# Kernel tuning notes

Measured on AMD Instinct MI355X. Metric: run time of the kernel, lower is better.

Reference implementation:

```python
import jax, jax.numpy as jnp
import numpy as np

CUTOFF = 3.5
EPS = 1e-7  # keras.backend.epsilon()


def triplet_indices(N):
    # All triplets (i, j, k) with j < k and j, k != i  -> [N, T, 3], T = (N-1)(N-2)/2
    idx = []
    for i in range(N):
        others = [a for a in range(N) if a != i]
        for a in range(len(others)):
            for b in range(a + 1, len(others)):
                idx.append((i, others[a], others[b]))
    T = (N - 1) * (N - 2) // 2
    return np.asarray(idx, dtype=np.int32).reshape(N, T, 3)


def f_C(distance):
    return 0.5 * jnp.cos(np.pi * distance / CUTOFF) + 0.5


def _he(key, shape):
    fan_in = shape[0]
    return jax.random.normal(key, shape, dtype=jnp.float32) * np.sqrt(2.0 / fan_in)


def setup_inputs() -> dict:
    key = jax.random.key(0)
    ks = jax.random.split(key, 10)
    B, N = 32, 32
    # build realistic symmetric distance matrices from random coordinates
    coords = jax.random.normal(ks[0], (B, N, 3), dtype=jnp.float32) * 2.0
    D = jnp.linalg.norm(coords[:, :, None, :] - coords[:, None, :, :], axis=-1)
    Z = jax.random.randint(ks[1], (B, N), 1, 10).astype(jnp.float32)
    dims = [(9, 64), (64, 64), (64, 64), (64, 64), (64, 64), (64, 128), (128, 256)]
    inp = {"distance_matrices": D, "num_species_batch": Z}
    for li, (fi, fo) in enumerate(dims):
        inp[f"W{li}"] = _he(ks[2 + li], (fi, fo))
        inp[f"b{li}"] = jnp.zeros((fo,), dtype=jnp.float32)
    return inp


def ang_mlp(x, W0, b0, W1, b1, W2, b2, W3, b3, W4, b4, W5, b5, W6, b6):
    x_res = jnp.tanh(x @ W0 + b0)
    h = jnp.tanh(x_res @ W1 + b1)
    blk1 = h + x_res
    h = jnp.tanh(blk1 @ W2 + b2)
    h = jnp.tanh(h @ W3 + b3)
    h = jnp.tanh(h @ W4 + b4)
    blk2 = h + blk1
    blk3 = jnp.tanh(blk2 @ W5 + b5)
    return jnp.tanh(blk3 @ W6 + b6)


def reference(distance_matrices, num_species_batch, W0, b0, W1, b1, W2, b2,
              W3, b3, W4, b4, W5, b5, W6, b6):
    D = distance_matrices          # [B, N, N]
    Z = num_species_batch          # [B, N]
    N = D.shape[1]
    trip = jnp.asarray(triplet_indices(N))          # [N, T, 3] static
    ti, tj, tk = trip[..., 0], trip[..., 1], trip[..., 2]   # each [N, T]

    # gather triplet distances / species -> [B, N, T]
    R_ij = D[:, ti, tj]
    R_ik = D[:, ti, tk]
    R_jk = D[:, tj, tk]
    z_i, z_j, z_k = Z[:, ti], Z[:, tj], Z[:, tk]

    # Carnot formula for angles
    def carnot(a, b, c):
        return (a ** 2 + b ** 2 - c ** 2) / jnp.maximum(2.0 * a * b, 1e-10)
    cos_i = carnot(R_ij, R_ik, R_jk)
    cos_j = carnot(R_ij, R_jk, R_ik)
    cos_k = carnot(R_ik, R_jk, R_ij)

    geo = jnp.stack([R_ij + R_ik + R_jk,
                     R_ij * R_ik + R_ij * R_jk + R_ik * R_jk,
                     R_ij * R_ik * R_jk], axis=-1)                      # [B,N,T,3]
    chem = jnp.stack([
        z_i + z_j + z_k,
        cos_i + cos_j + cos_k,
        z_i * (z_j + z_k) + z_j * z_k - cos_i * (cos_j + cos_k) - cos_j * cos_k,
        z_i * (cos_j + cos_k) + cos_i * (z_j + z_k) + z_j * cos_k + cos_j * z_k,
        z_i * (z_j * z_k - cos_j * cos_k) - cos_i * (z_j * cos_k + cos_j * z_k),
        z_i * (z_j * cos_k + cos_j * z_k) + cos_i * (z_j * z_k - cos_j * cos_k),
    ], axis=-1)                                                          # [B,N,T,6]
    geo = geo / (jnp.linalg.norm(geo, axis=-1, keepdims=True) + EPS)
    chem = chem / (jnp.linalg.norm(chem, axis=-1, keepdims=True) + EPS)
    mlp_in = jnp.concatenate([geo, chem], axis=-1)                       # [B,N,T,9]

    mlp_out = ang_mlp(mlp_in, W0, b0, W1, b1, W2, b2, W3, b3, W4, b4, W5, b5, W6, b6)  # [B,N,T,256]

    # cutoff smoothing; triplets with a central distance beyond the cutoff map to 0
    within = ((R_ij < CUTOFF) & (R_ik < CUTOFF)).astype(mlp_out.dtype)
    smooth = f_C(R_ij) * f_C(R_ik) * within                              # [B,N,T]
    aev = jnp.sum(mlp_out * smooth[..., None], axis=2)                   # [B,N,256]
    return aev
```

## Files before the change

kernel.cpp:

```cpp
#include <hip/hip_runtime.h>

namespace {

constexpr int T = 465;
constexpr int M = 31;
constexpr float FCUT = 3.5f;
constexpr float PI_OVER_CUT = 0.8975979010256552f;
constexpr int REC = 12;
constexpr int K2_BLOCKS = 512;
constexpr int MAXROWS_HARD = 1024 * 480;

constexpr int OFF_WB = 0;
constexpr int OFF_B  = 4096;
constexpr int OFF_A  = 8192;
constexpr int OFF_C  = 12288;
constexpr int OFF_F  = 16384;
constexpr int OFF_SM = 16960;
constexpr int OFF_CT = 17024;
constexpr int LDS_FLOATS = 17088;

__device__ __forceinline__ float ftanh(float x) {
    x = fminf(fmaxf(x, -15.0f), 15.0f);
    const float e = __expf(2.0f * x);
    return (e - 1.0f) * __builtin_amdgcn_rcpf(e + 1.0f);
}

__global__ __launch_bounds__(64, 1)
void feat_kernel(const float* __restrict__ D, const float* __restrict__ Z,
                 float* __restrict__ rows, int* __restrict__ ctr, int maxrows)
{
    const int lane = threadIdx.x;
    const int center = blockIdx.x;
    const int bi = center >> 5, i = center & 31;
    const float* __restrict__ Drow = D + bi * 1024;
    const float* __restrict__ Zrow = Z + bi * 32;
    const float z_i = Zrow[i];

    unsigned long long masks[8];
    int cnt = 0;
    #pragma unroll
    for (int rnd = 0; rnd < 8; ++rnd) {
        const int t = rnd * 64 + lane;
        bool act = false;
        if (t < T) {
            int a = 0, rem = t;
            while (rem >= M - 1 - a) { rem -= M - 1 - a; ++a; }
            const int b = a + 1 + rem;
            const int j = a + (a >= i);
            const int k = b + (b >= i);
            const float rij = Drow[i * 32 + j];
            const float rik = Drow[i * 32 + k];
            act = (rij < FCUT) && (rik < FCUT);
        }
        masks[rnd] = __ballot(act);
        cnt += (int)__popcll(masks[rnd]);
    }
    const int padded = (cnt + 15) & ~15;
    if (padded == 0) return;
    int base = 0;
    if (lane == 0) base = atomicAdd(ctr, padded);
    base = __shfl(base, 0);
    if (base + padded > maxrows) return;

    int pre = 0;
    #pragma unroll
    for (int rnd = 0; rnd < 8; ++rnd) {
        const unsigned long long mb = masks[rnd];
        const bool act = (mb >> lane) & 1ull;
        const int slot = base + pre + (int)__popcll(mb & ((1ull << lane) - 1ull));
        pre += (int)__popcll(mb);
        if (act) {
            const int t = rnd * 64 + lane;
            int a = 0, rem = t;
            while (rem >= M - 1 - a) { rem -= M - 1 - a; ++a; }
            const int b = a + 1 + rem;
            const int j = a + (a >= i);
            const int k = b + (b >= i);
            const float rij = Drow[i * 32 + j];
            const float rik = Drow[i * 32 + k];
            const float rjk = Drow[j * 32 + k];
            const float zj = Zrow[j], zk = Zrow[k];
            const float rij2 = rij * rij, rik2 = rik * rik, rjk2 = rjk * rjk;
            const float ci = (rij2 + rik2 - rjk2) / fmaxf(2.f * rij * rik, 1e-10f);
            const float cj = (rij2 + rjk2 - rik2) / fmaxf(2.f * rij * rjk, 1e-10f);
            const float ck = (rik2 + rjk2 - rij2) / fmaxf(2.f * rik * rjk, 1e-10f);
            const float g0 = rij + rik + rjk;
            const float g1 = rij * rik + rij * rjk + rik * rjk;
            const float g2 = rij * rik * rjk;
            const float rg = 1.0f / (sqrtf(g0 * g0 + g1 * g1 + g2 * g2) + 1e-7f);
            const float s0 = z_i + zj + zk;
            const float s1 = ci + cj + ck;
            const float s2 = z_i * (zj + zk) + zj * zk - ci * (cj + ck) - cj * ck;
            const float s3 = z_i * (cj + ck) + ci * (zj + zk) + zj * ck + cj * zk;
            const float s4 = z_i * (zj * zk - cj * ck) - ci * (zj * ck + cj * zk);
            const float s5 = z_i * (zj * ck + cj * zk) + ci * (zj * zk - cj * ck);
            const float rs = 1.0f / (sqrtf(s0*s0 + s1*s1 + s2*s2 + s3*s3 + s4*s4 + s5*s5) + 1e-7f);
            const float fij = 0.5f * cosf(PI_OVER_CUT * rij) + 0.5f;
            const float fik = 0.5f * cosf(PI_OVER_CUT * rik) + 0.5f;
            float4* dst = (float4*)(rows + (size_t)slot * REC);
            dst[0] = make_float4(g0 * rg, g1 * rg, g2 * rg, s0 * rs);
            dst[1] = make_float4(s1 * rs, s2 * rs, s3 * rs, s4 * rs);
            dst[2] = make_float4(s5 * rs, fij * fik, __int_as_float(center), 0.f);
        }
    }
    for (int p = cnt + lane; p < padded; p += 64) {
        float4* dst = (float4*)(rows + (size_t)(base + p) * REC);
        dst[0] = make_float4(0.f, 0.f, 0.f, 0.f);
        dst[1] = make_float4(0.f, 0.f, 0.f, 0.f);
        dst[2] = make_float4(0.f, 0.f, __int_as_float(center), 0.f);
    }
}

template<int INF>
__device__ __forceinline__ void stage_w(const float* __restrict__ W, int OUT, int c0,
                                        float* __restrict__ wb, int t)
{
    constexpr int TOT = INF * 64 / 4;
    #pragma unroll 1
    for (int idx = t; idx < TOT; idx += 256) {
        const int f = idx * 4;
        const int kk = f >> 6;
        const int c = f & 63;
        *(float4*)(wb + f) = *(const float4*)(W + (size_t)kk * OUT + c0 + c);
    }
}

template<int INF>
__device__ __forceinline__ void accum(const float* __restrict__ wb,
                                      const float* __restrict__ xin,
                                      int lane, int wcol, float acc[16])
{
    #pragma unroll 4
    for (int kk = 0; kk < INF; ++kk) {
        const float x = xin[kk * 64 + lane];
        const float* wr = wb + kk * 64 + wcol;
        const float4 w0 = *(const float4*)(wr + 0);
        const float4 w1 = *(const float4*)(wr + 4);
        const float4 w2 = *(const float4*)(wr + 8);
        const float4 w3 = *(const float4*)(wr + 12);
        acc[ 0] = fmaf(x, w0.x, acc[ 0]);  acc[ 1] = fmaf(x, w0.y, acc[ 1]);
        acc[ 2] = fmaf(x, w0.z, acc[ 2]);  acc[ 3] = fmaf(x, w0.w, acc[ 3]);
        acc[ 4] = fmaf(x, w1.x, acc[ 4]);  acc[ 5] = fmaf(x, w1.y, acc[ 5]);
        acc[ 6] = fmaf(x, w1.z, acc[ 6]);  acc[ 7] = fmaf(x, w1.w, acc[ 7]);
        acc[ 8] = fmaf(x, w2.x, acc[ 8]);  acc[ 9] = fmaf(x, w2.y, acc[ 9]);
        acc[10] = fmaf(x, w2.z, acc[10]);  acc[11] = fmaf(x, w2.w, acc[11]);
        acc[12] = fmaf(x, w3.x, acc[12]);  acc[13] = fmaf(x, w3.y, acc[13]);
        acc[14] = fmaf(x, w3.z, acc[14]);  acc[15] = fmaf(x, w3.w, acc[15]);
    }
}

__device__ __forceinline__ void bias_init(const float* __restrict__ Bp, int off,
                                          float acc[16])
{
    const float4 b0 = *(const float4*)(Bp + off + 0);
    const float4 b1 = *(const float4*)(Bp + off + 4);
    const float4 b2 = *(const float4*)(Bp + off + 8);
    const float4 b3 = *(const float4*)(Bp + off + 12);
    acc[0]=b0.x; acc[1]=b0.y; acc[2]=b0.z; acc[3]=b0.w;
    acc[4]=b1.x; acc[5]=b1.y; acc[6]=b1.z; acc[7]=b1.w;
    acc[8]=b2.x; acc[9]=b2.y; acc[10]=b2.z; acc[11]=b2.w;
    acc[12]=b3.x; acc[13]=b3.y; acc[14]=b3.z; acc[15]=b3.w;
}

__global__ __launch_bounds__(256, 2)
void mlp_kernel(const float* __restrict__ rows, const int* __restrict__ ctr,
                const float* __restrict__ W0, const float* __restrict__ B0,
                const float* __restrict__ W1, const float* __restrict__ B1,
                const float* __restrict__ W2, const float* __restrict__ B2,
                const float* __restrict__ W3, const float* __restrict__ B3,
                const float* __restrict__ W4, const float* __restrict__ B4,
                const float* __restrict__ W5, const float* __restrict__ B5,
                const float* __restrict__ W6, const float* __restrict__ B6,
                float* __restrict__ out, int maxrows)
{
    __shared__ float lds[LDS_FLOATS];
    float* __restrict__ WB = lds + OFF_WB;
    float* __restrict__ Bb = lds + OFF_B;
    float* __restrict__ Ab = lds + OFF_A;
    float* __restrict__ Cb = lds + OFF_C;
    float* __restrict__ Fb = lds + OFF_F;
    float* __restrict__ SMb = lds + OFF_SM;
    int*   __restrict__ CTb = (int*)(lds + OFF_CT);

    const int t = threadIdx.x;
    const int lane = t & 63;
    const int wcol = (t >> 6) * 16;
    int nrows = *ctr;
    if (nrows > maxrows) nrows = maxrows & ~15;

    for (int tile = blockIdx.x; tile * 64 < nrows; tile += K2_BLOCKS) {
        __syncthreads();
        if (t < 64) {
            const int r = tile * 64 + t;
            float4 v0 = make_float4(0,0,0,0), v1 = v0, v2 = v0;
            if (r < nrows) {
                const float4* rec = (const float4*)(rows + (size_t)r * REC);
                v0 = rec[0]; v1 = rec[1]; v2 = rec[2];
            } else {
                v2.z = __int_as_float(-1);
            }
            Fb[0*64+t]=v0.x; Fb[1*64+t]=v0.y; Fb[2*64+t]=v0.z;
            Fb[3*64+t]=v0.w; Fb[4*64+t]=v1.x; Fb[5*64+t]=v1.y;
            Fb[6*64+t]=v1.z; Fb[7*64+t]=v1.w; Fb[8*64+t]=v2.x;
            SMb[t] = v2.y;
            CTb[t] = __float_as_int(v2.z);
        }
        stage_w<9>(W0, 64, 0, WB, t);
        __syncthreads();

        float acc[16];

        bias_init(B0, wcol, acc);
        accum<9>(WB, Fb, lane, wcol, acc);
        #pragma unroll
        for (int q = 0; q < 16; ++q) Ab[(wcol + q) * 64 + lane] = ftanh(acc[q]);

        __syncthreads();
        stage_w<64>(W1, 64, 0, WB, t);
        __syncthreads();
        bias_init(B1, wcol, acc);
        accum<64>(WB, Ab, lane, wcol, acc);
        #pragma unroll
        for (int q = 0; q < 16; ++q) {
            const int f = (wcol + q) * 64 + lane;
            Bb[f] = ftanh(acc[q]) + Ab[f];
        }

        __syncthreads();
        stage_w<64>(W2, 64, 0, WB, t);
        __syncthreads();
        bias_init(B2, wcol, acc);
        accum<64>(WB, Bb, lane, wcol, acc);
        #pragma unroll
        for (int q = 0; q < 16; ++q) Cb[(wcol + q) * 64 + lane] = ftanh(acc[q]);

        __syncthreads();
        stage_w<64>(W3, 64, 0, WB, t);
        __syncthreads();
        bias_init(B3, wcol, acc);
        accum<64>(WB, Cb, lane, wcol, acc);
        #pragma unroll
        for (int q = 0; q < 16; ++q) Ab[(wcol + q) * 64 + lane] = ftanh(acc[q]);

        __syncthreads();
        stage_w<64>(W4, 64, 0, WB, t);
        __syncthreads();
        bias_init(B4, wcol, acc);
        accum<64>(WB, Ab, lane, wcol, acc);
        #pragma unroll
        for (int q = 0; q < 16; ++q) {
            const int f = (wcol + q) * 64 + lane;
            Bb[f] = ftanh(acc[q]) + Bb[f];
        }

        __syncthreads();
        stage_w<64>(W5, 128, 0, WB, t);
        __syncthreads();
        bias_init(B5, wcol, acc);
        accum<64>(WB, Bb, lane, wcol, acc);
        #pragma unroll
        for (int q = 0; q < 16; ++q) Ab[(wcol + q) * 64 + lane] = ftanh(acc[q]);

        __syncthreads();
        stage_w<64>(W5, 128, 64, WB, t);
        __syncthreads();
        bias_init(B5, 64 + wcol, acc);
        accum<64>(WB, Bb, lane, wcol, acc);
        #pragma unroll
        for (int q = 0; q < 16; ++q) Cb[(wcol + q) * 64 + lane] = ftanh(acc[q]);

        const float sm = SMb[lane];
        const int ct = CTb[lane];
        #pragma unroll 1
        for (int c0 = 0; c0 < 256; c0 += 64) {
            __syncthreads();
            stage_w<128>(W6, 256, c0, lds, t);
            __syncthreads();
            float a6[16];
            bias_init(B6, c0 + wcol, a6);
            accum<64>(lds, Ab, lane, wcol, a6);
            accum<64>(lds + 64 * 64, Cb, lane, wcol, a6);
            #pragma unroll
            for (int q = 0; q < 16; ++q) {
                float v = ftanh(a6[q]) * sm;
                v += __shfl_xor(v, 1);
                v += __shfl_xor(v, 2);
                v += __shfl_xor(v, 4);
                v += __shfl_xor(v, 8);
                if (((lane & 15) == 0) && ct >= 0)
                    atomicAdd(out + (size_t)ct * 256 + c0 + wcol + q, v);
            }
        }
    }
}

}

extern "C" void kernel_launch(void* const* d_in, const int* in_sizes, int n_in,
                              void* d_out, int out_size, void* d_ws, size_t ws_size,
                              hipStream_t stream) {
    (void)in_sizes; (void)n_in;

    const float* D  = (const float*)d_in[0];
    const float* Z  = (const float*)d_in[1];
    const float* W0 = (const float*)d_in[2];  const float* B0 = (const float*)d_in[3];
    const float* W1 = (const float*)d_in[4];  const float* B1 = (const float*)d_in[5];
    const float* W2 = (const float*)d_in[6];  const float* B2 = (const float*)d_in[7];
    const float* W3 = (const float*)d_in[8];  const float* B3 = (const float*)d_in[9];
    const float* W4 = (const float*)d_in[10]; const float* B4 = (const float*)d_in[11];
    const float* W5 = (const float*)d_in[12]; const float* B5 = (const float*)d_in[13];
    const float* W6 = (const float*)d_in[14]; const float* B6 = (const float*)d_in[15];
    float* out = (float*)d_out;

    int* ctr = (int*)d_ws;
    float* rowbuf = (float*)((char*)d_ws + 64);
    size_t avail = (ws_size > 64) ? (ws_size - 64) / (REC * sizeof(float)) : 0;
    int maxrows = (int)((avail < (size_t)MAXROWS_HARD) ? avail : (size_t)MAXROWS_HARD);

    hipMemsetAsync(d_ws, 0, 64, stream);
    hipMemsetAsync(d_out, 0, sizeof(float) * (size_t)out_size, stream);

    feat_kernel<<<1024, 64, 0, stream>>>(D, Z, rowbuf, ctr, maxrows);
    mlp_kernel<<<K2_BLOCKS, 256, 0, stream>>>(rowbuf, ctr,
                                              W0, B0, W1, B1, W2, B2, W3, B3,
                                              W4, B4, W5, B5, W6, B6, out, maxrows);
}
```

Baseline: 412.9 us.

## Read MLP weights via scalar constant loads instead of staging through LDS

Removes the per-layer staging of weight tiles into shared memory and the barriers around it. Each wave instead reads its 16-column weight slice straight from global memory through the constant address space, with a wave-uniform column index (readfirstlane) so the loads can become scalar loads. The smaller LDS footprint and a launch bound of 3 blocks per CU aim to raise occupancy. In exchange, every k step issues scalar memory loads that depend on the scalar cache, which may add latency compared with LDS reads.

```diff
diff --git a/kernel.cpp b/kernel.cpp
--- a/kernel.cpp
+++ b/kernel.cpp
@@ -10,14 +10,8 @@
 constexpr int K2_BLOCKS = 512;
 constexpr int MAXROWS_HARD = 1024 * 480;
 
-constexpr int OFF_WB = 0;
-constexpr int OFF_B  = 4096;
-constexpr int OFF_A  = 8192;
-constexpr int OFF_C  = 12288;
-constexpr int OFF_F  = 16384;
-constexpr int OFF_SM = 16960;
-constexpr int OFF_CT = 17024;
-constexpr int LDS_FLOATS = 17088;
+typedef float __attribute__((ext_vector_type(4))) f4v;
+typedef const __attribute__((address_space(4))) f4v* cf4p;
 
 __device__ __forceinline__ float ftanh(float x) {
     x = fminf(fmaxf(x, -15.0f), 15.0f);
@@ -111,33 +105,19 @@
     }
 }
 
-template<int INF>
-__device__ __forceinline__ void stage_w(const float* __restrict__ W, int OUT, int c0,
-                                        float* __restrict__ wb, int t)
+template<int INF, int LDW>
+__device__ __forceinline__ void accum_s(const float* Wcol,
+                                        const float* __restrict__ xin,
+                                        int lane, float acc[16])
 {
-    constexpr int TOT = INF * 64 / 4;
-    #pragma unroll 1
-    for (int idx = t; idx < TOT; idx += 256) {
-        const int f = idx * 4;
-        const int kk = f >> 6;
-        const int c = f & 63;
-        *(float4*)(wb + f) = *(const float4*)(W + (size_t)kk * OUT + c0 + c);
-    }
-}
-
-template<int INF>
-__device__ __forceinline__ void accum(const float* __restrict__ wb,
-                                      const float* __restrict__ xin,
-                                      int lane, int wcol, float acc[16])
-{
-    #pragma unroll 4
+    cf4p w = (cf4p)(uintptr_t)Wcol;
+    #pragma unroll 2
     for (int kk = 0; kk < INF; ++kk) {
+        const f4v w0 = w[kk * (LDW / 4) + 0];
+        const f4v w1 = w[kk * (LDW / 4) + 1];
+        const f4v w2 = w[kk * (LDW / 4) + 2];
+        const f4v w3 = w[kk * (LDW / 4) + 3];
         const float x = xin[kk * 64 + lane];
-        const float* wr = wb + kk * 64 + wcol;
-        const float4 w0 = *(const float4*)(wr + 0);
-        const float4 w1 = *(const float4*)(wr + 4);
-        const float4 w2 = *(const float4*)(wr + 8);
-        const float4 w3 = *(const float4*)(wr + 12);
         acc[ 0] = fmaf(x, w0.x, acc[ 0]);  acc[ 1] = fmaf(x, w0.y, acc[ 1]);
         acc[ 2] = fmaf(x, w0.z, acc[ 2]);  acc[ 3] = fmaf(x, w0.w, acc[ 3]);
         acc[ 4] = fmaf(x, w1.x, acc[ 4]);  acc[ 5] = fmaf(x, w1.y, acc[ 5]);
@@ -149,20 +129,16 @@
     }
 }
 
-__device__ __forceinline__ void bias_init(const float* __restrict__ Bp, int off,
-                                          float acc[16])
-{
-    const float4 b0 = *(const float4*)(Bp + off + 0);
-    const float4 b1 = *(const float4*)(Bp + off + 4);
-    const float4 b2 = *(const float4*)(Bp + off + 8);
-    const float4 b3 = *(const float4*)(Bp + off + 12);
+__device__ __forceinline__ void bias_s(const float* Bcol, float acc[16]) {
+    cf4p b = (cf4p)(uintptr_t)Bcol;
+    const f4v b0 = b[0], b1 = b[1], b2 = b[2], b3 = b[3];
     acc[0]=b0.x; acc[1]=b0.y; acc[2]=b0.z; acc[3]=b0.w;
     acc[4]=b1.x; acc[5]=b1.y; acc[6]=b1.z; acc[7]=b1.w;
     acc[8]=b2.x; acc[9]=b2.y; acc[10]=b2.z; acc[11]=b2.w;
     acc[12]=b3.x; acc[13]=b3.y; acc[14]=b3.z; acc[15]=b3.w;
 }
 
-__global__ __launch_bounds__(256, 2)
+__global__ __launch_bounds__(256, 3)
 void mlp_kernel(const float* __restrict__ rows, const int* __restrict__ ctr,
                 const float* __restrict__ W0, const float* __restrict__ B0,
                 const float* __restrict__ W1, const float* __restrict__ B1,
@@ -173,18 +149,17 @@
                 const float* __restrict__ W6, const float* __restrict__ B6,
                 float* __restrict__ out, int maxrows)
 {
-    __shared__ float lds[LDS_FLOATS];
-    float* __restrict__ WB = lds + OFF_WB;
-    float* __restrict__ Bb = lds + OFF_B;
-    float* __restrict__ Ab = lds + OFF_A;
-    float* __restrict__ Cb = lds + OFF_C;
-    float* __restrict__ Fb = lds + OFF_F;
-    float* __restrict__ SMb = lds + OFF_SM;
-    int*   __restrict__ CTb = (int*)(lds + OFF_CT);
+    __shared__ float Ab[64 * 64];
+    __shared__ float Bb[64 * 64];
+    __shared__ float Cb[64 * 64];
+    __shared__ float Fb[9 * 64];
+    __shared__ float SMb[64];
+    __shared__ int   CTb[64];
 
     const int t = threadIdx.x;
     const int lane = t & 63;
-    const int wcol = (t >> 6) * 16;
+    const int wcol = __builtin_amdgcn_readfirstlane((t >> 6) * 16);
+
     int nrows = *ctr;
     if (nrows > maxrows) nrows = maxrows & ~15;
 
@@ -205,81 +180,65 @@
             SMb[t] = v2.y;
             CTb[t] = __float_as_int(v2.z);
         }
-        stage_w<9>(W0, 64, 0, WB, t);
         __syncthreads();
 
         float acc[16];
 
-        bias_init(B0, wcol, acc);
-        accum<9>(WB, Fb, lane, wcol, acc);
+        bias_s(B0 + wcol, acc);
+        accum_s<9, 64>(W0 + wcol, Fb, lane, acc);
         #pragma unroll
         for (int q = 0; q < 16; ++q) Ab[(wcol + q) * 64 + lane] = ftanh(acc[q]);
-
-        __syncthreads();
-        stage_w<64>(W1, 64, 0, WB, t);
-        __syncthreads();
-        bias_init(B1, wcol, acc);
-        accum<64>(WB, Ab, lane, wcol, acc);
+        __syncthreads();
+
+        bias_s(B1 + wcol, acc);
+        accum_s<64, 64>(W1 + wcol, Ab, lane, acc);
         #pragma unroll
         for (int q = 0; q < 16; ++q) {
             const int f = (wcol + q) * 64 + lane;
             Bb[f] = ftanh(acc[q]) + Ab[f];
         }
-
-        __syncthreads();
-        stage_w<64>(W2, 64, 0, WB, t);
-        __syncthreads();
-        bias_init(B2, wcol, acc);
-        accum<64>(WB, Bb, lane, wcol, acc);
+        __syncthreads();
+
+        bias_s(B2 + wcol, acc);
+        accum_s<64, 64>(W2 + wcol, Bb, lane, acc);
         #pragma unroll
         for (int q = 0; q < 16; ++q) Cb[(wcol + q) * 64 + lane] = ftanh(acc[q]);
-
-        __syncthreads();
-        stage_w<64>(W3, 64, 0, WB, t);
-        __syncthreads();
-        bias_init(B3, wcol, acc);
-        accum<64>(WB, Cb, lane, wcol, acc);
+        __syncthreads();
+
+        bias_s(B3 + wcol, acc);
+        accum_s<64, 64>(W3 + wcol, Cb, lane, acc);
         #pragma unroll
         for (int q = 0; q < 16; ++q) Ab[(wcol + q) * 64 + lane] = ftanh(acc[q]);
-
-        __syncthreads();
-        stage_w<64>(W4, 64, 0, WB, t);
-        __syncthreads();
-        bias_init(B4, wcol, acc);
-        accum<64>(WB, Ab, lane, wcol, acc);
+        __syncthreads();
+
+        bias_s(B4 + wcol, acc);
+        accum_s<64, 64>(W4 + wcol, Ab, lane, acc);
         #pragma unroll
         for (int q = 0; q < 16; ++q) {
             const int f = (wcol + q) * 64 + lane;
             Bb[f] = ftanh(acc[q]) + Bb[f];
         }
-
-        __syncthreads();
-        stage_w<64>(W5, 128, 0, WB, t);
-        __syncthreads();
-        bias_init(B5, wcol, acc);
-        accum<64>(WB, Bb, lane, wcol, acc);
+        __syncthreads();
+
+        bias_s(B5 + wcol, acc);
+        accum_s<64, 128>(W5 + wcol, Bb, lane, acc);
         #pragma unroll
         for (int q = 0; q < 16; ++q) Ab[(wcol + q) * 64 + lane] = ftanh(acc[q]);
 
-        __syncthreads();
-        stage_w<64>(W5, 128, 64, WB, t);
-        __syncthreads();
-        bias_init(B5, 64 + wcol, acc);
-        accum<64>(WB, Bb, lane, wcol, acc);
+        bias_s(B5 + 64 + wcol, acc);
+        accum_s<64, 128>(W5 + 64 + wcol, Bb, lane, acc);
         #pragma unroll
         for (int q = 0; q < 16; ++q) Cb[(wcol + q) * 64 + lane] = ftanh(acc[q]);
+        __syncthreads();
 
         const float sm = SMb[lane];
         const int ct = CTb[lane];
         #pragma unroll 1
         for (int c0 = 0; c0 < 256; c0 += 64) {
-            __syncthreads();
-            stage_w<128>(W6, 256, c0, lds, t);
-            __syncthreads();
             float a6[16];
-            bias_init(B6, c0 + wcol, a6);
-            accum<64>(lds, Ab, lane, wcol, a6);
-            accum<64>(lds + 64 * 64, Cb, lane, wcol, a6);
+            bias_s(B6 + c0 + wcol, a6);
+            accum_s<64, 256>(W6 + c0 + wcol, Ab, lane, a6);
+            accum_s<64, 256>(W6 + 64 * 256 + c0 + wcol, Cb, lane, a6);
             #pragma unroll
             for (int q = 0; q < 16; ++q) {
                 float v = ftanh(a6[q]) * sm;
```

Result: slower. 560.1 us (+35.7%).
